# Kernel optimization log

Measured on AMD Instinct MI355X. Metric: run time of the kernel, lower is better.

The kernel has to match this reference:

```python
import jax, jax.numpy as jnp
import numpy as np

B, S, D_MODEL, HEADS = 2, 2048, 1024, 16
HEAD_DIM = D_MODEL // HEADS
NEG = -1.0e9


def setup_inputs() -> dict:
    key = jax.random.key(0)
    ks = jax.random.split(key, 7)
    query = jax.random.normal(ks[0], (B, S, D_MODEL), dtype=jnp.float32)
    k_in = jax.random.normal(ks[1], (B, S, D_MODEL), dtype=jnp.float32)
    value = jax.random.normal(ks[2], (B, S, D_MODEL), dtype=jnp.float32)
    # nn.Linear(d_model, d_model, bias=False) weights, torch layout [out, in]
    sc = 1.0 / np.sqrt(D_MODEL)
    Wq = jax.random.uniform(ks[3], (D_MODEL, D_MODEL), jnp.float32, -sc, sc)
    Wk = jax.random.uniform(ks[4], (D_MODEL, D_MODEL), jnp.float32, -sc, sc)
    Wv = jax.random.uniform(ks[5], (D_MODEL, D_MODEL), jnp.float32, -sc, sc)
    Wo = jax.random.uniform(ks[6], (D_MODEL, D_MODEL), jnp.float32, -sc, sc)
    # causal mask: 1 where attention allowed, 0 where masked
    mask = jnp.tril(jnp.ones((S, S), dtype=jnp.int32))[None, None]
    freqs_complex_form = jnp.zeros((1,), dtype=jnp.float32)  # unused by the module
    return {"query": query, "key": k_in, "value": value,
            "freqs_complex_form": freqs_complex_form, "mask": mask,
            "Wq": Wq, "Wk": Wk, "Wv": Wv, "Wo": Wo}


def reference(query, key, value, freqs_complex_form, mask, Wq, Wk, Wv, Wo):
    # QKV projections (torch Linear: y = x @ W.T)
    q = query @ Wq.T
    k = key @ Wk.T
    v = value @ Wv.T
    # [B, S, D] -> [B, H, S, Dh]
    q = q.reshape(B, S, HEADS, HEAD_DIM).transpose(0, 2, 1, 3)
    k = k.reshape(B, S, HEADS, HEAD_DIM).transpose(0, 2, 1, 3)
    v = v.reshape(B, S, HEADS, HEAD_DIM).transpose(0, 2, 1, 3)
    # scores [B, H, S, S]
    att = jnp.einsum('bhqd,bhkd->bhqk', q, k) / jnp.sqrt(jnp.float32(HEAD_DIM))
    att = jnp.where(mask == 0, NEG, att)
    att = jax.nn.softmax(att, axis=-1)
    # dropout is identity in eval / deterministic reference
    out = jnp.einsum('bhqk,bhkd->bhqd', att, v)
    out = out.transpose(0, 2, 1, 3).reshape(B, S, D_MODEL)
    return out @ Wo.T
```

## Files before the change

### kernel.cpp

```cpp
#include <hip/hip_runtime.h>

#define DM   1024
#define SEQ  2048
#define BATCH 2
#define NH   16
#define DHEAD 64
#define MTOT (BATCH*SEQ)
#define KVB  64
#define EOFF ((size_t)MTOT * DM)
#define NROW (BATCH * NH * SEQ)

typedef _Float16 half_t;
typedef _Float16 half4 __attribute__((ext_vector_type(4)));
typedef _Float16 half8 __attribute__((ext_vector_type(8)));
typedef float    floatx4 __attribute__((ext_vector_type(4)));

#define SCALE2 0.18033688f

__device__ __forceinline__ float fast_exp2(float x) {
  float r;
  asm volatile("v_exp_f32 %0, %1" : "=v"(r) : "v"(x));
  return r;
}

__device__ __forceinline__ void gload_lds16(const half_t* g, half_t* l) {
  __builtin_amdgcn_global_load_lds(
      (const __attribute__((address_space(1))) void*)g,
      (__attribute__((address_space(3))) void*)l, 16, 0, 0);
}

__global__ __launch_bounds__(256) void cvt_all(const float* __restrict__ q, const float* __restrict__ k,
                                               const float* __restrict__ v, const float* __restrict__ wq,
                                               const float* __restrict__ wk, const float* __restrict__ wv,
                                               const float* __restrict__ wo,
                                               half_t* __restrict__ dq, half_t* __restrict__ dk,
                                               half_t* __restrict__ dv, half_t* __restrict__ dwq,
                                               half_t* __restrict__ dwk, half_t* __restrict__ dwv,
                                               half_t* __restrict__ dwo) {
  const int y = blockIdx.y;
  const float* s; half_t* d; int n8;
  const int En8 = MTOT * DM / 8, Wn8 = DM * DM / 8;
  switch (y) {
    case 0: s = q;  d = dq;  n8 = En8; break;
    case 1: s = k;  d = dk;  n8 = En8; break;
    case 2: s = v;  d = dv;  n8 = En8; break;
    case 3: s = wq; d = dwq; n8 = Wn8; break;
    case 4: s = wk; d = dwk; n8 = Wn8; break;
    case 5: s = wv; d = dwv; n8 = Wn8; break;
    default: s = wo; d = dwo; n8 = Wn8; break;
  }
  int i = blockIdx.x * 256 + threadIdx.x;
  if (i >= n8) return;
  const float4* sp = reinterpret_cast<const float4*>(s);
  float4 u = sp[(size_t)i * 2], w = sp[(size_t)i * 2 + 1];
  half8 h;
  h[0] = (half_t)u.x; h[1] = (half_t)u.y; h[2] = (half_t)u.z; h[3] = (half_t)u.w;
  h[4] = (half_t)w.x; h[5] = (half_t)w.y; h[6] = (half_t)w.z; h[7] = (half_t)w.w;
  *reinterpret_cast<half8*>(d + (size_t)i * 8) = h;
}

__global__ __launch_bounds__(256) void gemm_qkv(const half_t* __restrict__ Xq,
                                                const half_t* __restrict__ Xk,
                                                const half_t* __restrict__ Xv,
                                                const half_t* __restrict__ Wq,
                                                const half_t* __restrict__ Wk,
                                                const half_t* __restrict__ Wv,
                                                half_t* __restrict__ Qb,
                                                half_t* __restrict__ Kb,
                                                half_t* __restrict__ Vb) {
  __shared__ half_t As[2][128 * 32];
  __shared__ half_t Bs[2][128 * 32];
  const int which = blockIdx.x >> 8;
  const int flat = blockIdx.x & 255;
  const half_t* Ag = (which == 0) ? Xq : (which == 1) ? Xk : Xv;
  const half_t* Bg = (which == 0) ? Wq : (which == 1) ? Wk : Wv;
  half_t* Cg       = (which == 0) ? Qb : (which == 1) ? Kb : Vb;
  const float esc  = (which == 0) ? SCALE2 : 1.0f;

  const int tid = threadIdx.x, lane = tid & 63, w = tid >> 6;
  const int lr = lane & 15, lg = lane >> 4;
  const int xcd = flat & 7, bi = flat >> 3;
  const int m0 = (xcd * 4 + (bi >> 3)) * 128;
  const int n0 = (bi & 7) * 128;
  const int wm = (w >> 1) * 64, wn = (w & 1) * 64;
  floatx4 acc[4][4] = {};

  const half_t* aSrc[2]; const half_t* bSrc[2]; int dstOff[2];
#pragma unroll
  for (int j = 0; j < 2; j++) {
    int id = tid + j * 256;
    aSrc[j] = Ag + (size_t)(m0 + (id >> 2)) * DM + (id & 3) * 8;
    bSrc[j] = Bg + (size_t)(n0 + (id >> 2)) * DM + (id & 3) * 8;
    dstOff[j] = id * 8;
  }

#define STAGE_QKV(BUF, K0)                                                    \
  {                                                                           \
    _Pragma("unroll")                                                         \
    for (int j = 0; j < 2; j++) {                                             \
      gload_lds16(aSrc[j] + (K0), &As[BUF][dstOff[j]]);                       \
      gload_lds16(bSrc[j] + (K0), &Bs[BUF][dstOff[j]]);                       \
    }                                                                         \
  }
#define COMP_QKV(BUF)                                                         \
  {                                                                           \
    half8 a[4], b[4];                                                         \
    _Pragma("unroll")                                                         \
    for (int i = 0; i < 4; i++)                                               \
      a[i] = *reinterpret_cast<half8*>(&As[BUF][(wm + i * 16 + lr) * 32 + lg * 8]); \
    _Pragma("unroll")                                                         \
    for (int j = 0; j < 4; j++)                                               \
      b[j] = *reinterpret_cast<half8*>(&Bs[BUF][(wn + j * 16 + lr) * 32 + lg * 8]); \
    _Pragma("unroll")                                                         \
    for (int i = 0; i < 4; i++)                                               \
      _Pragma("unroll")                                                       \
      for (int j = 0; j < 4; j++)                                             \
        acc[i][j] = __builtin_amdgcn_mfma_f32_16x16x32_f16(b[j], a[i], acc[i][j], 0, 0, 0); \
  }

  STAGE_QKV(0, 0);
  __syncthreads();
  int buf = 0;
#pragma unroll 1
  for (int t = 0; t < 31; t++) {
    STAGE_QKV(buf ^ 1, (t + 1) * 32);
    COMP_QKV(buf);
    __syncthreads();
    buf ^= 1;
  }
  COMP_QKV(buf);

#pragma unroll
  for (int i = 0; i < 4; i++) {
    const int m = m0 + wm + i * 16 + lr;
    const int b_ = m >> 11, s_ = m & 2047;
#pragma unroll
    for (int j = 0; j < 4; j++) {
      const int n = n0 + wn + j * 16 + lg * 4;
      const int h_ = n >> 6, d_ = n & 63;
      half4 o;
#pragma unroll
      for (int r = 0; r < 4; r++) o[r] = (half_t)(acc[i][j][r] * esc);
      *reinterpret_cast<half4*>(
          &Cg[(((size_t)b_ * NH + h_) * SEQ + s_) * DHEAD + d_]) = o;
    }
  }
#undef STAGE_QKV
#undef COMP_QKV
}

__global__ __launch_bounds__(256) void gemm_o(const half_t* __restrict__ Ag,
                                              const half_t* __restrict__ Bg,
                                              float* __restrict__ Cg) {
  __shared__ half_t As[2][128 * 32];
  __shared__ half_t Bs[2][64 * 32];
  const int tid = threadIdx.x, lane = tid & 63, w = tid >> 6;
  const int lr = lane & 15, lg = lane >> 4;
  const int flat = blockIdx.x;
  const int xcd = flat & 7, bi = flat >> 3;
  const int m0 = (xcd * 4 + (bi >> 4)) * 128;
  const int n0 = (bi & 15) * 64;
  const int wm = (w >> 1) * 64, wn = (w & 1) * 32;
  floatx4 acc[4][2] = {};

  const half_t* aSrc[2]; const half_t* bSrc; int dstOff[2];
#pragma unroll
  for (int j = 0; j < 2; j++) {
    int id = tid + j * 256;
    aSrc[j] = Ag + (size_t)(m0 + (id >> 2)) * DM + (id & 3) * 8;
    dstOff[j] = id * 8;
  }
  bSrc = Bg + (size_t)(n0 + (tid >> 2)) * DM + (tid & 3) * 8;

#define STAGE_O(BUF, K0)                                                      \
  {                                                                           \
    _Pragma("unroll")                                                         \
    for (int j = 0; j < 2; j++)                                               \
      gload_lds16(aSrc[j] + (K0), &As[BUF][dstOff[j]]);                       \
    gload_lds16(bSrc + (K0), &Bs[BUF][tid * 8]);                              \
  }
#define COMP_O(BUF)                                                           \
  {                                                                           \
    half8 a[4], b[2];                                                         \
    _Pragma("unroll")                                                         \
    for (int i = 0; i < 4; i++)                                               \
      a[i] = *reinterpret_cast<half8*>(&As[BUF][(wm + i * 16 + lr) * 32 + lg * 8]); \
    _Pragma("unroll")                                                         \
    for (int j = 0; j < 2; j++)                                               \
      b[j] = *reinterpret_cast<half8*>(&Bs[BUF][(wn + j * 16 + lr) * 32 + lg * 8]); \
    _Pragma("unroll")                                                         \
    for (int i = 0; i < 4; i++)                                               \
      _Pragma("unroll")                                                       \
      for (int j = 0; j < 2; j++)                                             \
        acc[i][j] = __builtin_amdgcn_mfma_f32_16x16x32_f16(b[j], a[i], acc[i][j], 0, 0, 0); \
  }

  STAGE_O(0, 0);
  __syncthreads();
  int buf = 0;
#pragma unroll 1
  for (int t = 0; t < 31; t++) {
    STAGE_O(buf ^ 1, (t + 1) * 32);
    COMP_O(buf);
    __syncthreads();
    buf ^= 1;
  }
  COMP_O(buf);

#pragma unroll
  for (int i = 0; i < 4; i++) {
    const int m = m0 + wm + i * 16 + lr;
#pragma unroll
    for (int j = 0; j < 2; j++) {
      const int n = n0 + wn + j * 16 + lg * 4;
      floatx4 o = acc[i][j];
      *reinterpret_cast<floatx4*>(&Cg[(size_t)m * DM + n]) = o;
    }
  }
#undef STAGE_O
#undef COMP_O
}

__global__ __launch_bounds__(512) void attn_fwd(const half_t* __restrict__ Q,
                                                const half_t* __restrict__ K,
                                                const half_t* __restrict__ V,
                                                half_t* __restrict__ P,
                                                float* __restrict__ L) {
  __shared__ half_t Ks[64][72];
  __shared__ half_t Vt[80][72];
  const int tid = threadIdx.x, lane = tid & 63, w = tid >> 6;
  const int lr = lane & 15, lg = lane >> 4;

  const int flat = blockIdx.x;
  const int xcd = flat & 7, idx = flat >> 3;
  const int qblk = 15 - (idx >> 3);
  const int sub = idx & 7;
  const int combo = xcd * 4 + (sub >> 1);
  const int split = sub & 1;
  const int h = combo & 15, b = combo >> 4;

  const size_t bh = ((size_t)b * NH + h) * SEQ * DHEAD;
  const int q0 = qblk * 128 + w * 16;
  const int nt = 2 * (qblk + 1);
  const int h0 = qblk + 1;
  const int t0 = split ? h0 : 0;
  const int t1 = split ? nt : h0;

  for (int i2 = tid; i2 < 16 * 72; i2 += 512) {
    int d = i2 / 72, kv = i2 % 72;
    Vt[64 + d][kv] = (d == 0) ? (half_t)1.0f : (half_t)0.0f;
  }

  half8 qf[2];
#pragma unroll
  for (int ks = 0; ks < 2; ks++)
    qf[ks] = *reinterpret_cast<const half8*>(
        Q + bh + (size_t)(q0 + lr) * DHEAD + ks * 32 + lg * 8);

  floatx4 accO[5] = {};

  half8 kr, vr;
#define LOADT(t)                                                              \
  {                                                                           \
    const int kvb2 = (t) * KVB;                                               \
    kr = *reinterpret_cast<const half8*>(                                     \
        K + bh + (size_t)(kvb2 + (tid >> 3)) * DHEAD + (tid & 7) * 8);        \
    vr = *reinterpret_cast<const half8*>(                                     \
        V + bh + (size_t)(kvb2 + (tid & 63)) * DHEAD + (tid >> 6) * 8);       \
  }
#define WRITET()                                                              \
  {                                                                           \
    *reinterpret_cast<half8*>(&Ks[tid >> 3][(tid & 7) * 8]) = kr;             \
    int vrow = tid & 63, vcol = (tid >> 6) * 8;                               \
    _Pragma("unroll")                                                         \
    for (int e = 0; e < 8; e++) Vt[vcol + e][vrow] = vr[e];                   \
  }

  LOADT(t0);
  WRITET();
  __syncthreads();

#pragma unroll 1
  for (int t = t0; t < t1; t++) {
    const int kvbase = t * KVB;
    if (t + 1 < t1) LOADT(t + 1);
    if (kvbase <= q0 + 15) {
      const bool need_mask = (kvbase + KVB - 1) > q0;
      floatx4 s[4];
#pragma unroll
      for (int jt = 0; jt < 4; jt++) {
        floatx4 a0 = {};
#pragma unroll
        for (int ks = 0; ks < 2; ks++) {
          half8 ak = *reinterpret_cast<half8*>(&Ks[jt * 16 + lr][ks * 32 + lg * 8]);
          a0 = __builtin_amdgcn_mfma_f32_16x16x32_f16(ak, qf[ks], a0, 0, 0, 0);
        }
        s[jt] = a0;
      }
      const int qq = q0 + lr;
#pragma unroll
      for (int jt = 0; jt < 4; jt++)
#pragma unroll
        for (int r = 0; r < 4; r++) {
          float pp = fast_exp2(s[jt][r]);
          if (need_mask) {
            int kv = kvbase + jt * 16 + lg * 4 + r;
            if (kv > qq) pp = 0.f;
          }
          s[jt][r] = pp;
        }
      half8 pb[2];
#pragma unroll
      for (int ks = 0; ks < 2; ks++) {
#pragma unroll
        for (int e = 0; e < 4; e++) {
          pb[ks][e]     = (half_t)s[2 * ks][e];
          pb[ks][4 + e] = (half_t)s[2 * ks + 1][e];
        }
      }
#pragma unroll
      for (int j = 0; j < 5; j++) {
#pragma unroll
        for (int ks = 0; ks < 2; ks++) {
          half4 x = *reinterpret_cast<half4*>(&Vt[j * 16 + lr][ks * 32 + lg * 4]);
          half4 y = *reinterpret_cast<half4*>(&Vt[j * 16 + lr][ks * 32 + 16 + lg * 4]);
          half8 av;
          av[0] = x[0]; av[1] = x[1]; av[2] = x[2]; av[3] = x[3];
          av[4] = y[0]; av[5] = y[1]; av[6] = y[2]; av[7] = y[3];
          accO[j] = __builtin_amdgcn_mfma_f32_16x16x32_f16(av, pb[ks], accO[j], 0, 0, 0);
        }
      }
    }
    if (t + 1 < t1) {
      __syncthreads();
      WRITET();
      __syncthreads();
    }
  }

  half_t* Pw = P + (size_t)split * EOFF;
  float*  Lw = L + (size_t)split * NROW;
  {
    const int q = q0 + lr;
    const size_t rowbase = bh + (size_t)q * DHEAD;
#pragma unroll
    for (int j = 0; j < 4; j++) {
      half4 o;
#pragma unroll
      for (int r = 0; r < 4; r++) o[r] = (half_t)accO[j][r];
      *reinterpret_cast<half4*>(&Pw[rowbase + j * 16 + lg * 4]) = o;
    }
    if (lg == 0)
      Lw[((size_t)b * NH + h) * SEQ + q] = accO[4][0];
  }
#undef LOADT
#undef WRITET
}

__global__ __launch_bounds__(256) void attn_combine(const half_t* __restrict__ P,
                                                    const float* __restrict__ L,
                                                    half_t* __restrict__ Ab) {
  size_t i = (size_t)blockIdx.x * 256 + threadIdx.x;
  half8 p0 = *reinterpret_cast<const half8*>(P + i * 8);
  half8 p1 = *reinterpret_cast<const half8*>(P + EOFF + i * 8);
  size_t row = i >> 3;
  float l = L[row] + L[NROW + row];
  float inv = 1.0f / l;
  int s_ = (int)(row % SEQ);
  int h_ = (int)((row / SEQ) % NH);
  int b_ = (int)(row / ((size_t)SEQ * NH));
  int d0 = (int)(i & 7) * 8;
  half8 o;
#pragma unroll
  for (int e = 0; e < 8; e++)
    o[e] = (half_t)(((float)p0[e] + (float)p1[e]) * inv);
  *reinterpret_cast<half8*>(Ab + ((size_t)b_ * SEQ + s_) * DM + h_ * DHEAD + d0) = o;
}

extern "C" void kernel_launch(void* const* d_in, const int* in_sizes, int n_in,
                              void* d_out, int out_size, void* d_ws, size_t ws_size,
                              hipStream_t stream) {
  const float* q_in = (const float*)d_in[0];
  const float* k_in = (const float*)d_in[1];
  const float* v_in = (const float*)d_in[2];
  const float* Wq   = (const float*)d_in[5];
  const float* Wk   = (const float*)d_in[6];
  const float* Wv   = (const float*)d_in[7];
  const float* Wo   = (const float*)d_in[8];

  const size_t E = EOFF;
  const size_t W = (size_t)DM * DM;
  half_t* ws  = (half_t*)d_ws;
  half_t* Xq  = ws;
  half_t* Xk  = ws + E;
  half_t* Xv  = ws + 2 * E;
  half_t* Wqh = ws + 3 * E;
  half_t* Wkh = Wqh + W;
  half_t* Wvh = Wkh + W;
  half_t* Woh = Wvh + W;
  half_t* Qb  = ws + 4 * E;
  half_t* Kb  = ws + 5 * E;
  half_t* Vb  = ws + 6 * E;
  half_t* Ab  = Xq;
  half_t* Pp  = Xk;
  float*  Lp  = (float*)Wqh;
  if (ws_size < 7 * E * sizeof(half_t)) return;

  cvt_all<<<dim3(2048, 7), 256, 0, stream>>>(q_in, k_in, v_in, Wq, Wk, Wv, Wo,
                                             Xq, Xk, Xv, Wqh, Wkh, Wvh, Woh);
  gemm_qkv<<<768, 256, 0, stream>>>(Xq, Xk, Xv, Wqh, Wkh, Wvh, Qb, Kb, Vb);
  attn_fwd<<<1024, 512, 0, stream>>>(Qb, Kb, Vb, Pp, Lp);
  attn_combine<<<2048, 256, 0, stream>>>(Pp, Lp, Ab);
  gemm_o<<<512, 256, 0, stream>>>(Ab, Woh, (float*)d_out);
}
```

Baseline: 129.2 us.

## Fuse split-KV attention combine into output projection GEMM A-tile loading

Drops the separate attn_combine kernel. gemm_o now reads the two partial attention outputs and their row sums directly, normalises them in registers and writes the fp16 A tile to shared memory. Register staging replaces the async global-to-LDS copy for A. This removes one launch and the round trip of the combined activation through global memory. In exchange the A-operand loads become synchronous register loads that are recomputed per N-tile, so each column block re-reads both partials plus a reciprocal, and LDS stores may add latency to the GEMM loop.

```diff
diff --git a/kernel.cpp b/kernel.cpp
--- a/kernel.cpp
+++ b/kernel.cpp
@@ -149,7 +149,8 @@
 #undef COMP_QKV
 }
 
-__global__ __launch_bounds__(256) void gemm_o(const half_t* __restrict__ Ag,
+__global__ __launch_bounds__(256) void gemm_o(const half_t* __restrict__ Pp,
+                                              const float* __restrict__ Lp,
                                               const half_t* __restrict__ Bg,
                                               float* __restrict__ Cg) {
   __shared__ half_t As[2][128 * 32];
@@ -163,21 +164,43 @@
   const int wm = (w >> 1) * 64, wn = (w & 1) * 32;
   floatx4 acc[4][2] = {};
 
-  const half_t* aSrc[2]; const half_t* bSrc; int dstOff[2];
+  size_t rowterm[2]; int col8[2], dst[2];
 #pragma unroll
   for (int j = 0; j < 2; j++) {
     int id = tid + j * 256;
-    aSrc[j] = Ag + (size_t)(m0 + (id >> 2)) * DM + (id & 3) * 8;
-    dstOff[j] = id * 8;
-  }
-  bSrc = Bg + (size_t)(n0 + (tid >> 2)) * DM + (tid & 3) * 8;
-
-#define STAGE_O(BUF, K0)                                                      \
-  {                                                                           \
-    _Pragma("unroll")                                                         \
-    for (int j = 0; j < 2; j++)                                               \
-      gload_lds16(aSrc[j] + (K0), &As[BUF][dstOff[j]]);                       \
-    gload_lds16(bSrc + (K0), &Bs[BUF][tid * 8]);                              \
+    int row = m0 + (id >> 2);
+    col8[j] = (id & 3) * 8;
+    dst[j] = id * 8;
+    int b_ = row >> 11, s_ = row & 2047;
+    rowterm[j] = (size_t)b_ * NH * SEQ + s_;
+  }
+  const half_t* bSrc = Bg + (size_t)(n0 + (tid >> 2)) * DM + (tid & 3) * 8;
+
+  half8 p0r[2], p1r[2];
+  float invv[2];
+
+#define LOADP(K0)                                                             \
+  {                                                                           \
+    _Pragma("unroll")                                                         \
+    for (int j = 0; j < 2; j++) {                                             \
+      int k = (K0) + col8[j];                                                 \
+      size_t lrow = rowterm[j] + (size_t)(k >> 6) * SEQ;                      \
+      size_t pbase = lrow * 64 + (k & 63);                                    \
+      p0r[j] = *reinterpret_cast<const half8*>(Pp + pbase);                   \
+      p1r[j] = *reinterpret_cast<const half8*>(Pp + EOFF + pbase);            \
+      invv[j] = 1.0f / (Lp[lrow] + Lp[NROW + lrow]);                          \
+    }                                                                         \
+  }
+#define WRITEP(BUF)                                                           \
+  {                                                                           \
+    _Pragma("unroll")                                                         \
+    for (int j = 0; j < 2; j++) {                                             \
+      half8 o;                                                                \
+      _Pragma("unroll")                                                       \
+      for (int e = 0; e < 8; e++)                                             \
+        o[e] = (half_t)(((float)p0r[j][e] + (float)p1r[j][e]) * invv[j]);     \
+      *reinterpret_cast<half8*>(&As[BUF][dst[j]]) = o;                        \
+    }                                                                         \
   }
 #define COMP_O(BUF)                                                           \
   {                                                                           \
@@ -195,13 +218,18 @@
         acc[i][j] = __builtin_amdgcn_mfma_f32_16x16x32_f16(b[j], a[i], acc[i][j], 0, 0, 0); \
   }
 
-  STAGE_O(0, 0);
+  LOADP(0);
+  gload_lds16(bSrc, &Bs[0][tid * 8]);
+  WRITEP(0);
   __syncthreads();
   int buf = 0;
 #pragma unroll 1
   for (int t = 0; t < 31; t++) {
-    STAGE_O(buf ^ 1, (t + 1) * 32);
+    const int k0 = (t + 1) * 32;
+    gload_lds16(bSrc + k0, &Bs[buf ^ 1][tid * 8]);
+    LOADP(k0);
     COMP_O(buf);
+    WRITEP(buf ^ 1);
     __syncthreads();
     buf ^= 1;
   }
@@ -217,7 +245,8 @@
       *reinterpret_cast<floatx4*>(&Cg[(size_t)m * DM + n]) = o;
     }
   }
-#undef STAGE_O
+#undef LOADP
+#undef WRITEP
 #undef COMP_O
 }
 
@@ -357,26 +386,6 @@
 #undef WRITET
 }
 
-__global__ __launch_bounds__(256) void attn_combine(const half_t* __restrict__ P,
-                                                    const float* __restrict__ L,
-                                                    half_t* __restrict__ Ab) {
-  size_t i = (size_t)blockIdx.x * 256 + threadIdx.x;
-  half8 p0 = *reinterpret_cast<const half8*>(P + i * 8);
-  half8 p1 = *reinterpret_cast<const half8*>(P + EOFF + i * 8);
-  size_t row = i >> 3;
-  float l = L[row] + L[NROW + row];
-  float inv = 1.0f / l;
-  int s_ = (int)(row % SEQ);
-  int h_ = (int)((row / SEQ) % NH);
-  int b_ = (int)(row / ((size_t)SEQ * NH));
-  int d0 = (int)(i & 7) * 8;
-  half8 o;
-#pragma unroll
-  for (int e = 0; e < 8; e++)
-    o[e] = (half_t)(((float)p0[e] + (float)p1[e]) * inv);
-  *reinterpret_cast<half8*>(Ab + ((size_t)b_ * SEQ + s_) * DM + h_ * DHEAD + d0) = o;
-}
-
 extern "C" void kernel_launch(void* const* d_in, const int* in_sizes, int n_in,
                               void* d_out, int out_size, void* d_ws, size_t ws_size,
                               hipStream_t stream) {
@@ -401,7 +410,6 @@
   half_t* Qb  = ws + 4 * E;
   half_t* Kb  = ws + 5 * E;
   half_t* Vb  = ws + 6 * E;
-  half_t* Ab  = Xq;
   half_t* Pp  = Xk;
   float*  Lp  = (float*)Wqh;
   if (ws_size < 7 * E * sizeof(half_t)) return;
@@ -410,6 +418,5 @@
                                              Xq, Xk, Xv, Wqh, Wkh, Wvh, Woh);
   gemm_qkv<<<768, 256, 0, stream>>>(Xq, Xk, Xv, Wqh, Wkh, Wvh, Qb, Kb, Vb);
   attn_fwd<<<1024, 512, 0, stream>>>(Qb, Kb, Vb, Pp, Lp);
-  attn_combine<<<2048, 256, 0, stream>>>(Pp, Lp, Ab);
-  gemm_o<<<512, 256, 0, stream>>>(Ab, Woh, (float*)d_out);
-}
+  gemm_o<<<512, 256, 0, stream>>>(Pp, Lp, Woh, (float*)d_out);
+}
```

New measurement: 137.3 us. +6.2%, slower.
